# Optimization experiments

Hardware: AMD Instinct MI355X
Metric: run time of the kernel (lower is better)

Reference implementation:

```python
import jax, jax.numpy as jnp
import numpy as np

N, P, K, H, W = 16, 2048, 512, 256, 256
ZTHRESH = 2.0          # PRUN_ZSCORE_THRESHOLD
MULT = 5               # HV_HYPOTHESIS_IN_MASK_MULTIPLIER


def setup_inputs() -> dict:
    key = jax.random.key(0)
    uv_img = jax.random.normal(key, (N, 2, H, W), dtype=jnp.float32)
    rng = np.random.default_rng(0)
    # mask points per instance (torch.where(mask[i]) made fixed-shape)
    pts = rng.integers(0, H, size=(N, P, 2)).astype(np.int32)
    # multinomial pair sampling without replacement: distinct indices per pair
    i0 = rng.integers(0, P, size=(N, K))
    off = rng.integers(1, P, size=(N, K))
    i1 = (i0 + off) % P
    pair_idx = np.stack([i0, i1], axis=-1).astype(np.int32)
    return {"uv_img": uv_img, "pts": jnp.asarray(pts), "pair_idx": jnp.asarray(pair_idx)}


def _gather_uv(uv_img, coords):
    # uv_img: [N,2,H,W], coords: [N,M,2] int -> [N,M,2] uv values
    n, _, h, w = uv_img.shape
    flat = coords[..., 0] * w + coords[..., 1]            # [N,M]
    uv_flat = uv_img.reshape(n, 2, h * w)                 # [N,2,HW]
    g = jnp.take_along_axis(uv_flat, flat[:, None, :], axis=2)  # [N,2,M]
    return jnp.transpose(g, (0, 2, 1))                    # [N,M,2]


def reference(uv_img, pts, pair_idx):
    # --- generate hypotheses (batched pinverse solver) ---
    p0 = jnp.take_along_axis(pts, pair_idx[..., 0:1], axis=1)  # [N,K,2]
    p1 = jnp.take_along_axis(pts, pair_idx[..., 1:2], axis=1)  # [N,K,2]
    uv0 = _gather_uv(uv_img, p0)                               # [N,K,2]
    uv1 = _gather_uv(uv_img, p1)                               # [N,K,2]
    A = jnp.stack((uv0, -uv1), axis=-1)                        # [N,K,2,2]
    Bv = (p1 - p0).astype(jnp.float32)[..., None]              # [N,K,2,1]  (-p0 + p1)
    X = jnp.matmul(jnp.linalg.pinv(A), Bv)                     # [N,K,2,1]
    x0 = X[:, :, 0, :]                                         # [N,K,1]
    Y = x0 * uv0 + p0.astype(jnp.float32)                      # [N,K,2] hypotheses

    # --- prune outliers (z-score, drop -> nan in torch; here masked) ---
    mean = jnp.mean(Y, axis=1, keepdims=True)
    std = jnp.std(Y, axis=1, keepdims=True, ddof=1)
    z = jnp.abs((Y - mean) / std)
    bad = jnp.any(z > ZTHRESH, axis=-1) | jnp.any(jnp.isnan(Y), axis=-1)  # [N,K]
    Yz = jnp.where(bad[..., None], 0.0, Y)                     # nan-hypotheses zeroed (as torch does)

    # --- hypothesis weights ---
    ptsf = pts.astype(jnp.float32)                             # [N,P,2]
    uv_p = _gather_uv(uv_img, pts)                             # [N,P,2]
    d = Y[:, :, None, :] - ptsf[:, None, :, :]                 # [N,K,P,2]
    a = d / jnp.linalg.norm(d, axis=-1, keepdims=True)
    b = jnp.einsum('nkpc,npc->nkp', a, uv_p) > 0               # direction agreement
    w = jnp.sum(b, axis=-1)                                    # [N,K] int
    match = Y.astype(jnp.int32)[:, :, None, :] == pts[:, None, :, :]
    h_in_mask = jnp.sum(match[..., 0] & match[..., 1], axis=-1)  # [N,K]
    factor = jnp.where(h_in_mask == 1, MULT, 1)
    w = (factor * w).astype(jnp.float32)
    w = jnp.where(bad, 0.0, w)                                 # outlier rows get 0 weight
    w = w / jnp.maximum(jnp.sum(w, axis=1, keepdims=True), 1.0)

    weighted_mean = jnp.sum(Yz * w[..., None], axis=1)         # [N,2]
    pixel_xy = weighted_mean[:, ::-1]                          # (row,col) -> (x,y)
    return pixel_xy
```

## Files before the change

kernel.cpp:

```cpp
#include <hip/hip_runtime.h>
#include <math.h>

#define N_ 16
#define P_ 2048
#define K_ 512
#define H_ 256
#define W_ 256
#define ZTHRESH_ 2.0f

__global__ __launch_bounds__(256) void k1_gather(
    const float* __restrict__ uv_img, const int* __restrict__ pts,
    const int* __restrict__ pair, float* __restrict__ Y,
    float* __restrict__ uvp) {
  int id = blockIdx.x * 256 + threadIdx.x;
  if (id < N_ * P_) {
    int n = id / P_, p = id % P_;
    int c0 = pts[(n * P_ + p) * 2 + 0];
    int c1 = pts[(n * P_ + p) * 2 + 1];
    const float* base = uv_img + (size_t)n * 2 * H_ * W_;
    uvp[(n * P_ + p) * 2 + 0] = base[c0 * W_ + c1];
    uvp[(n * P_ + p) * 2 + 1] = base[H_ * W_ + c0 * W_ + c1];
  } else {
    int j = id - N_ * P_;
    if (j < N_ * K_) {
      int n = j / K_, k = j % K_;
      int i0 = pair[(n * K_ + k) * 2 + 0];
      int i1 = pair[(n * K_ + k) * 2 + 1];
      int p0y = pts[(n * P_ + i0) * 2 + 0], p0x = pts[(n * P_ + i0) * 2 + 1];
      int p1y = pts[(n * P_ + i1) * 2 + 0], p1x = pts[(n * P_ + i1) * 2 + 1];
      const float* base = uv_img + (size_t)n * 2 * H_ * W_;
      float u00 = base[p0y * W_ + p0x];
      float u01 = base[H_ * W_ + p0y * W_ + p0x];
      float u10 = base[p1y * W_ + p1x];
      float u11 = base[H_ * W_ + p1y * W_ + p1x];
      float B0 = (float)(p1y - p0y);
      float B1 = (float)(p1x - p0x);
      float det = u10 * u01 - u00 * u11;
      float x0 = (u10 * B1 - B0 * u11) / det;
      Y[(n * K_ + k) * 2 + 0] = x0 * u00 + (float)p0y;
      Y[(n * K_ + k) * 2 + 1] = x0 * u01 + (float)p0x;
    }
  }
}

__global__ __launch_bounds__(512) void k2_stats(
    const float* __restrict__ Y, int* __restrict__ bad,
    int* __restrict__ wcnt, int* __restrict__ hcnt) {
  int n = blockIdx.x;
  int tid = threadIdx.x;
  float y0 = Y[(n * K_ + tid) * 2 + 0];
  float y1 = Y[(n * K_ + tid) * 2 + 1];
  wcnt[n * K_ + tid] = 0;
  hcnt[n * K_ + tid] = 0;

  __shared__ float lds[8][2];
  __shared__ float mean0s, mean1s, std0s, std1s;
  int wave = tid >> 6, lane = tid & 63;

  float a0 = y0, a1 = y1;
  for (int off = 32; off >= 1; off >>= 1) {
    a0 += __shfl_down(a0, off);
    a1 += __shfl_down(a1, off);
  }
  if (lane == 0) { lds[wave][0] = a0; lds[wave][1] = a1; }
  __syncthreads();
  if (tid == 0) {
    float t0 = 0.f, t1 = 0.f;
    for (int i = 0; i < 8; i++) { t0 += lds[i][0]; t1 += lds[i][1]; }
    mean0s = t0 / (float)K_;
    mean1s = t1 / (float)K_;
  }
  __syncthreads();
  float m0 = mean0s, m1 = mean1s;
  float e0 = y0 - m0, e1 = y1 - m1;

  a0 = e0 * e0; a1 = e1 * e1;
  for (int off = 32; off >= 1; off >>= 1) {
    a0 += __shfl_down(a0, off);
    a1 += __shfl_down(a1, off);
  }
  __syncthreads();
  if (lane == 0) { lds[wave][0] = a0; lds[wave][1] = a1; }
  __syncthreads();
  if (tid == 0) {
    float t0 = 0.f, t1 = 0.f;
    for (int i = 0; i < 8; i++) { t0 += lds[i][0]; t1 += lds[i][1]; }
    std0s = sqrtf(t0 / (float)(K_ - 1));
    std1s = sqrtf(t1 / (float)(K_ - 1));
  }
  __syncthreads();
  float z0 = fabsf(e0 / std0s), z1 = fabsf(e1 / std1s);
  int b = (z0 > ZTHRESH_) | (z1 > ZTHRESH_) | (y0 != y0) | (y1 != y1);
  bad[n * K_ + tid] = b;
}

__global__ __launch_bounds__(256) void k3_votes(
    const float* __restrict__ Y, const int* __restrict__ pts,
    const float* __restrict__ uvp, int* __restrict__ wcnt,
    int* __restrict__ hcnt) {
  int b = blockIdx.x;
  int n = b >> 4;
  int kt = (b >> 3) & 1;
  int pt = b & 7;
  int tid = threadIdx.x;

  __shared__ float4 sf[256];
  __shared__ int2 si[256];

  int p = pt * 256 + tid;
  int py = pts[(n * P_ + p) * 2 + 0];
  int px = pts[(n * P_ + p) * 2 + 1];
  float u = uvp[(n * P_ + p) * 2 + 0];
  float v = uvp[(n * P_ + p) * 2 + 1];
  sf[tid] = make_float4((float)py, (float)px, u, v);
  si[tid] = make_int2(py, px);
  __syncthreads();

  int k = kt * 256 + tid;
  float y0 = Y[(n * K_ + k) * 2 + 0];
  float y1 = Y[(n * K_ + k) * 2 + 1];
  int iy0 = (int)y0, iy1 = (int)y1;
  int cnt = 0, hm = 0;
#pragma unroll 4
  for (int i = 0; i < 256; i++) {
    float4 f = sf[i];
    int2 ii = si[i];
    float d0 = y0 - f.x;
    float d1 = y1 - f.y;
    float dot = d0 * f.z + d1 * f.w;
    cnt += (dot > 0.f) ? 1 : 0;
    hm += ((iy0 == ii.x) & (iy1 == ii.y)) ? 1 : 0;
  }
  atomicAdd(&wcnt[n * K_ + k], cnt);
  atomicAdd(&hcnt[n * K_ + k], hm);
}

__global__ __launch_bounds__(512) void k4_out(
    const float* __restrict__ Y, const int* __restrict__ bad,
    const int* __restrict__ wcnt, const int* __restrict__ hcnt,
    float* __restrict__ out) {
  int n = blockIdx.x;
  int tid = threadIdx.x;
  float y0 = Y[(n * K_ + tid) * 2 + 0];
  float y1 = Y[(n * K_ + tid) * 2 + 1];
  int bd = bad[n * K_ + tid];
  float w = (float)wcnt[n * K_ + tid];
  if (hcnt[n * K_ + tid] == 1) w *= 5.0f;
  if (bd) w = 0.f;
  float yz0 = bd ? 0.f : y0;
  float yz1 = bd ? 0.f : y1;
  float sw = w, s0 = w * yz0, s1 = w * yz1;

  int wave = tid >> 6, lane = tid & 63;
  __shared__ float lds[8][3];
  for (int off = 32; off >= 1; off >>= 1) {
    sw += __shfl_down(sw, off);
    s0 += __shfl_down(s0, off);
    s1 += __shfl_down(s1, off);
  }
  if (lane == 0) { lds[wave][0] = sw; lds[wave][1] = s0; lds[wave][2] = s1; }
  __syncthreads();
  if (tid == 0) {
    float tw = 0.f, t0 = 0.f, t1 = 0.f;
    for (int i = 0; i < 8; i++) {
      tw += lds[i][0]; t0 += lds[i][1]; t1 += lds[i][2];
    }
    float denom = fmaxf(tw, 1.0f);
    out[n * 2 + 0] = t1 / denom;
    out[n * 2 + 1] = t0 / denom;
  }
}

extern "C" void kernel_launch(void* const* d_in, const int* in_sizes, int n_in,
                              void* d_out, int out_size, void* d_ws,
                              size_t ws_size, hipStream_t stream) {
  const float* uv_img = (const float*)d_in[0];
  const int* pts = (const int*)d_in[1];
  const int* pair = (const int*)d_in[2];
  float* out = (float*)d_out;

  float* Y = (float*)d_ws;
  float* uvp = Y + N_ * K_ * 2;
  int* bad = (int*)(uvp + N_ * P_ * 2);
  int* wcnt = bad + N_ * K_;
  int* hcnt = wcnt + N_ * K_;

  hipLaunchKernelGGL(k1_gather, dim3((N_ * P_ + N_ * K_) / 256), dim3(256), 0,
                     stream, uv_img, pts, pair, Y, uvp);
  hipLaunchKernelGGL(k2_stats, dim3(N_), dim3(K_), 0, stream, Y, bad, wcnt,
                     hcnt);
  hipLaunchKernelGGL(k3_votes, dim3(256), dim3(256), 0, stream, Y, pts, uvp,
                     wcnt, hcnt);
  hipLaunchKernelGGL(k4_out, dim3(N_), dim3(K_), 0, stream, Y, bad, wcnt, hcnt,
                     out);
}
```

Before: 26.55 us.

## Fuse four kernels into two with a last-block-done final reduction

The gather, z-score stats, vote counting and final weighted mean were four launches; they become two. Zeroing of the counters and done flags moves into the gather kernel. The stats blocks now run next to the vote blocks in one grid, and the last of each instance's 17 blocks, found through an atomic counter, does the final reduction. This removes two launch and serialization gaps, at the cost of threadfence and atomic overhead and more complex synchronization.

Result: slower. 38.60 us (+45.3%).

```diff
diff --git a/kernel.cpp b/kernel.cpp
--- a/kernel.cpp
+++ b/kernel.cpp
@@ -8,166 +8,177 @@
 #define W_ 256
 #define ZTHRESH_ 2.0f
 
-__global__ __launch_bounds__(256) void k1_gather(
+__global__ __launch_bounds__(256) void kA(
     const float* __restrict__ uv_img, const int* __restrict__ pts,
     const int* __restrict__ pair, float* __restrict__ Y,
-    float* __restrict__ uvp) {
+    float* __restrict__ uvp, int* __restrict__ wcnt, int* __restrict__ hcnt,
+    int* __restrict__ done) {
   int id = blockIdx.x * 256 + threadIdx.x;
   if (id < N_ * P_) {
-    int n = id / P_, p = id % P_;
-    int c0 = pts[(n * P_ + p) * 2 + 0];
-    int c1 = pts[(n * P_ + p) * 2 + 1];
+    int n = id >> 11, p = id & (P_ - 1);
+    int2 c = ((const int2*)pts)[n * P_ + p];
     const float* base = uv_img + (size_t)n * 2 * H_ * W_;
-    uvp[(n * P_ + p) * 2 + 0] = base[c0 * W_ + c1];
-    uvp[(n * P_ + p) * 2 + 1] = base[H_ * W_ + c0 * W_ + c1];
-  } else {
-    int j = id - N_ * P_;
-    if (j < N_ * K_) {
-      int n = j / K_, k = j % K_;
-      int i0 = pair[(n * K_ + k) * 2 + 0];
-      int i1 = pair[(n * K_ + k) * 2 + 1];
-      int p0y = pts[(n * P_ + i0) * 2 + 0], p0x = pts[(n * P_ + i0) * 2 + 1];
-      int p1y = pts[(n * P_ + i1) * 2 + 0], p1x = pts[(n * P_ + i1) * 2 + 1];
-      const float* base = uv_img + (size_t)n * 2 * H_ * W_;
-      float u00 = base[p0y * W_ + p0x];
-      float u01 = base[H_ * W_ + p0y * W_ + p0x];
-      float u10 = base[p1y * W_ + p1x];
-      float u11 = base[H_ * W_ + p1y * W_ + p1x];
-      float B0 = (float)(p1y - p0y);
-      float B1 = (float)(p1x - p0x);
-      float det = u10 * u01 - u00 * u11;
-      float x0 = (u10 * B1 - B0 * u11) / det;
-      Y[(n * K_ + k) * 2 + 0] = x0 * u00 + (float)p0y;
-      Y[(n * K_ + k) * 2 + 1] = x0 * u01 + (float)p0x;
-    }
-  }
+    float2 g;
+    g.x = base[c.x * W_ + c.y];
+    g.y = base[H_ * W_ + c.x * W_ + c.y];
+    ((float2*)uvp)[n * P_ + p] = g;
+    return;
+  }
+  id -= N_ * P_;
+  if (id < N_ * K_) {
+    int n = id >> 9, k = id & (K_ - 1);
+    int2 pr = ((const int2*)pair)[n * K_ + k];
+    int2 p0 = ((const int2*)pts)[n * P_ + pr.x];
+    int2 p1 = ((const int2*)pts)[n * P_ + pr.y];
+    const float* base = uv_img + (size_t)n * 2 * H_ * W_;
+    float u00 = base[p0.x * W_ + p0.y];
+    float u01 = base[H_ * W_ + p0.x * W_ + p0.y];
+    float u10 = base[p1.x * W_ + p1.y];
+    float u11 = base[H_ * W_ + p1.x * W_ + p1.y];
+    float B0 = (float)(p1.x - p0.x);
+    float B1 = (float)(p1.y - p0.y);
+    float det = u10 * u01 - u00 * u11;
+    float x0 = (u10 * B1 - B0 * u11) / det;
+    float2 y;
+    y.x = x0 * u00 + (float)p0.x;
+    y.y = x0 * u01 + (float)p0.y;
+    ((float2*)Y)[n * K_ + k] = y;
+    return;
+  }
+  id -= N_ * K_;
+  if (id < N_ * K_) {
+    wcnt[id] = 0;
+    hcnt[id] = 0;
+    return;
+  }
+  id -= N_ * K_;
+  if (id < N_) done[id] = 0;
 }
 
-__global__ __launch_bounds__(512) void k2_stats(
-    const float* __restrict__ Y, int* __restrict__ bad,
-    int* __restrict__ wcnt, int* __restrict__ hcnt) {
-  int n = blockIdx.x;
-  int tid = threadIdx.x;
-  float y0 = Y[(n * K_ + tid) * 2 + 0];
-  float y1 = Y[(n * K_ + tid) * 2 + 1];
-  wcnt[n * K_ + tid] = 0;
-  hcnt[n * K_ + tid] = 0;
-
-  __shared__ float lds[8][2];
-  __shared__ float mean0s, mean1s, std0s, std1s;
-  int wave = tid >> 6, lane = tid & 63;
-
-  float a0 = y0, a1 = y1;
-  for (int off = 32; off >= 1; off >>= 1) {
-    a0 += __shfl_down(a0, off);
-    a1 += __shfl_down(a1, off);
-  }
-  if (lane == 0) { lds[wave][0] = a0; lds[wave][1] = a1; }
-  __syncthreads();
-  if (tid == 0) {
-    float t0 = 0.f, t1 = 0.f;
-    for (int i = 0; i < 8; i++) { t0 += lds[i][0]; t1 += lds[i][1]; }
-    mean0s = t0 / (float)K_;
-    mean1s = t1 / (float)K_;
-  }
-  __syncthreads();
-  float m0 = mean0s, m1 = mean1s;
-  float e0 = y0 - m0, e1 = y1 - m1;
-
-  a0 = e0 * e0; a1 = e1 * e1;
-  for (int off = 32; off >= 1; off >>= 1) {
-    a0 += __shfl_down(a0, off);
-    a1 += __shfl_down(a1, off);
-  }
-  __syncthreads();
-  if (lane == 0) { lds[wave][0] = a0; lds[wave][1] = a1; }
-  __syncthreads();
-  if (tid == 0) {
-    float t0 = 0.f, t1 = 0.f;
-    for (int i = 0; i < 8; i++) { t0 += lds[i][0]; t1 += lds[i][1]; }
-    std0s = sqrtf(t0 / (float)(K_ - 1));
-    std1s = sqrtf(t1 / (float)(K_ - 1));
-  }
-  __syncthreads();
-  float z0 = fabsf(e0 / std0s), z1 = fabsf(e1 / std1s);
-  int b = (z0 > ZTHRESH_) | (z1 > ZTHRESH_) | (y0 != y0) | (y1 != y1);
-  bad[n * K_ + tid] = b;
-}
-
-__global__ __launch_bounds__(256) void k3_votes(
-    const float* __restrict__ Y, const int* __restrict__ pts,
-    const float* __restrict__ uvp, int* __restrict__ wcnt,
-    int* __restrict__ hcnt) {
-  int b = blockIdx.x;
-  int n = b >> 4;
-  int kt = (b >> 3) & 1;
-  int pt = b & 7;
-  int tid = threadIdx.x;
-
+__global__ __launch_bounds__(256) void kB(
+    const int* __restrict__ pts, const float* __restrict__ Y,
+    const float* __restrict__ uvp, int* __restrict__ bad,
+    int* __restrict__ wcnt, int* __restrict__ hcnt, int* __restrict__ done,
+    float* __restrict__ out) {
+  int b = blockIdx.x, tid = threadIdx.x;
   __shared__ float4 sf[256];
   __shared__ int2 si[256];
-
-  int p = pt * 256 + tid;
-  int py = pts[(n * P_ + p) * 2 + 0];
-  int px = pts[(n * P_ + p) * 2 + 1];
-  float u = uvp[(n * P_ + p) * 2 + 0];
-  float v = uvp[(n * P_ + p) * 2 + 1];
-  sf[tid] = make_float4((float)py, (float)px, u, v);
-  si[tid] = make_int2(py, px);
+  __shared__ float red[4][3];
+  __shared__ float m0s, m1s, sd0s, sd1s;
+  __shared__ int s_old;
+  int wave = tid >> 6, lane = tid & 63;
+  int n;
+
+  if (b < 256) {
+    n = b >> 4;
+    int kt = (b >> 3) & 1, pt = b & 7;
+    int p = pt * 256 + tid;
+    int2 pc = ((const int2*)pts)[n * P_ + p];
+    float2 uc = ((const float2*)uvp)[n * P_ + p];
+    sf[tid] = make_float4((float)pc.x, (float)pc.y, uc.x, uc.y);
+    si[tid] = pc;
+    __syncthreads();
+
+    int k = kt * 256 + tid;
+    float2 y = ((const float2*)Y)[n * K_ + k];
+    int iy0 = (int)y.x, iy1 = (int)y.y;
+    int cnt = 0, hm = 0;
+#pragma unroll 4
+    for (int i = 0; i < 256; i++) {
+      float4 f = sf[i];
+      int2 ii = si[i];
+      float d0 = y.x - f.x;
+      float d1 = y.y - f.y;
+      float dot = d0 * f.z + d1 * f.w;
+      cnt += (dot > 0.f) ? 1 : 0;
+      hm += ((iy0 == ii.x) & (iy1 == ii.y)) ? 1 : 0;
+    }
+    atomicAdd(&wcnt[n * K_ + k], cnt);
+    atomicAdd(&hcnt[n * K_ + k], hm);
+  } else {
+    n = b - 256;
+    float2 ya = ((const float2*)Y)[n * K_ + tid];
+    float2 yb = ((const float2*)Y)[n * K_ + tid + 256];
+    float a0 = ya.x + yb.x, a1 = ya.y + yb.y;
+    for (int off = 32; off >= 1; off >>= 1) {
+      a0 += __shfl_down(a0, off);
+      a1 += __shfl_down(a1, off);
+    }
+    if (lane == 0) { red[wave][0] = a0; red[wave][1] = a1; }
+    __syncthreads();
+    if (tid == 0) {
+      float t0 = red[0][0] + red[1][0] + red[2][0] + red[3][0];
+      float t1 = red[0][1] + red[1][1] + red[2][1] + red[3][1];
+      m0s = t0 / (float)K_;
+      m1s = t1 / (float)K_;
+    }
+    __syncthreads();
+    float m0 = m0s, m1 = m1s;
+    float ea0 = ya.x - m0, ea1 = ya.y - m1;
+    float eb0 = yb.x - m0, eb1 = yb.y - m1;
+    a0 = ea0 * ea0 + eb0 * eb0;
+    a1 = ea1 * ea1 + eb1 * eb1;
+    for (int off = 32; off >= 1; off >>= 1) {
+      a0 += __shfl_down(a0, off);
+      a1 += __shfl_down(a1, off);
+    }
+    __syncthreads();
+    if (lane == 0) { red[wave][0] = a0; red[wave][1] = a1; }
+    __syncthreads();
+    if (tid == 0) {
+      float t0 = red[0][0] + red[1][0] + red[2][0] + red[3][0];
+      float t1 = red[0][1] + red[1][1] + red[2][1] + red[3][1];
+      sd0s = sqrtf(t0 / (float)(K_ - 1));
+      sd1s = sqrtf(t1 / (float)(K_ - 1));
+    }
+    __syncthreads();
+    float sd0 = sd0s, sd1 = sd1s;
+    int bda = (fabsf(ea0 / sd0) > ZTHRESH_) | (fabsf(ea1 / sd1) > ZTHRESH_) |
+              (ya.x != ya.x) | (ya.y != ya.y);
+    int bdb = (fabsf(eb0 / sd0) > ZTHRESH_) | (fabsf(eb1 / sd1) > ZTHRESH_) |
+              (yb.x != yb.x) | (yb.y != yb.y);
+    bad[n * K_ + tid] = bda;
+    bad[n * K_ + tid + 256] = bdb;
+  }
+
+  __threadfence();
   __syncthreads();
-
-  int k = kt * 256 + tid;
-  float y0 = Y[(n * K_ + k) * 2 + 0];
-  float y1 = Y[(n * K_ + k) * 2 + 1];
-  int iy0 = (int)y0, iy1 = (int)y1;
-  int cnt = 0, hm = 0;
-#pragma unroll 4
-  for (int i = 0; i < 256; i++) {
-    float4 f = sf[i];
-    int2 ii = si[i];
-    float d0 = y0 - f.x;
-    float d1 = y1 - f.y;
-    float dot = d0 * f.z + d1 * f.w;
-    cnt += (dot > 0.f) ? 1 : 0;
-    hm += ((iy0 == ii.x) & (iy1 == ii.y)) ? 1 : 0;
-  }
-  atomicAdd(&wcnt[n * K_ + k], cnt);
-  atomicAdd(&hcnt[n * K_ + k], hm);
-}
-
-__global__ __launch_bounds__(512) void k4_out(
-    const float* __restrict__ Y, const int* __restrict__ bad,
-    const int* __restrict__ wcnt, const int* __restrict__ hcnt,
-    float* __restrict__ out) {
-  int n = blockIdx.x;
-  int tid = threadIdx.x;
-  float y0 = Y[(n * K_ + tid) * 2 + 0];
-  float y1 = Y[(n * K_ + tid) * 2 + 1];
-  int bd = bad[n * K_ + tid];
-  float w = (float)wcnt[n * K_ + tid];
-  if (hcnt[n * K_ + tid] == 1) w *= 5.0f;
-  if (bd) w = 0.f;
-  float yz0 = bd ? 0.f : y0;
-  float yz1 = bd ? 0.f : y1;
-  float sw = w, s0 = w * yz0, s1 = w * yz1;
-
-  int wave = tid >> 6, lane = tid & 63;
-  __shared__ float lds[8][3];
-  for (int off = 32; off >= 1; off >>= 1) {
-    sw += __shfl_down(sw, off);
-    s0 += __shfl_down(s0, off);
-    s1 += __shfl_down(s1, off);
-  }
-  if (lane == 0) { lds[wave][0] = sw; lds[wave][1] = s0; lds[wave][2] = s1; }
+  if (tid == 0)
+    s_old = __hip_atomic_fetch_add(&done[n], 1, __ATOMIC_ACQ_REL,
+                                   __HIP_MEMORY_SCOPE_AGENT);
   __syncthreads();
-  if (tid == 0) {
-    float tw = 0.f, t0 = 0.f, t1 = 0.f;
-    for (int i = 0; i < 8; i++) {
-      tw += lds[i][0]; t0 += lds[i][1]; t1 += lds[i][2];
-    }
-    float denom = fmaxf(tw, 1.0f);
-    out[n * 2 + 0] = t1 / denom;
-    out[n * 2 + 1] = t0 / denom;
+  if (s_old == 16) {
+    float sw = 0.f, s0 = 0.f, s1 = 0.f;
+    for (int kk = tid; kk < K_; kk += 256) {
+      float2 y = ((const float2*)Y)[n * K_ + kk];
+      int bd = __hip_atomic_load(&bad[n * K_ + kk], __ATOMIC_RELAXED,
+                                 __HIP_MEMORY_SCOPE_AGENT);
+      int wc = __hip_atomic_load(&wcnt[n * K_ + kk], __ATOMIC_RELAXED,
+                                 __HIP_MEMORY_SCOPE_AGENT);
+      int hc = __hip_atomic_load(&hcnt[n * K_ + kk], __ATOMIC_RELAXED,
+                                 __HIP_MEMORY_SCOPE_AGENT);
+      float w = (float)wc * ((hc == 1) ? 5.0f : 1.0f);
+      if (bd) w = 0.f;
+      sw += w;
+      s0 += w * (bd ? 0.f : y.x);
+      s1 += w * (bd ? 0.f : y.y);
+    }
+    for (int off = 32; off >= 1; off >>= 1) {
+      sw += __shfl_down(sw, off);
+      s0 += __shfl_down(s0, off);
+      s1 += __shfl_down(s1, off);
+    }
+    __syncthreads();
+    if (lane == 0) { red[wave][0] = sw; red[wave][1] = s0; red[wave][2] = s1; }
+    __syncthreads();
+    if (tid == 0) {
+      float tw = red[0][0] + red[1][0] + red[2][0] + red[3][0];
+      float t0 = red[0][1] + red[1][1] + red[2][1] + red[3][1];
+      float t1 = red[0][2] + red[1][2] + red[2][2] + red[3][2];
+      float den = fmaxf(tw, 1.0f);
+      out[n * 2 + 0] = t1 / den;
+      out[n * 2 + 1] = t0 / den;
+    }
   }
 }
 
@@ -184,13 +195,11 @@
   int* bad = (int*)(uvp + N_ * P_ * 2);
   int* wcnt = bad + N_ * K_;
   int* hcnt = wcnt + N_ * K_;
-
-  hipLaunchKernelGGL(k1_gather, dim3((N_ * P_ + N_ * K_) / 256), dim3(256), 0,
-                     stream, uv_img, pts, pair, Y, uvp);
-  hipLaunchKernelGGL(k2_stats, dim3(N_), dim3(K_), 0, stream, Y, bad, wcnt,
-                     hcnt);
-  hipLaunchKernelGGL(k3_votes, dim3(256), dim3(256), 0, stream, Y, pts, uvp,
-                     wcnt, hcnt);
-  hipLaunchKernelGGL(k4_out, dim3(N_), dim3(K_), 0, stream, Y, bad, wcnt, hcnt,
-                     out);
+  int* done = hcnt + N_ * K_;
+
+  int itemsA = N_ * P_ + N_ * K_ + N_ * K_ + N_;
+  hipLaunchKernelGGL(kA, dim3((itemsA + 255) / 256), dim3(256), 0, stream,
+                     uv_img, pts, pair, Y, uvp, wcnt, hcnt, done);
+  hipLaunchKernelGGL(kB, dim3(272), dim3(256), 0, stream, pts, Y, uvp, bad,
+                     wcnt, hcnt, done, out);
 }
```

## Fuse gather, stats, voting and reduction into one kernel plus tiny final

Applied to the files above, without the earlier changes.

Replaces four kernels with a main kernel where each block recomputes all hypotheses and z-score stats for its instance in LDS, then votes for its 32-hypothesis slice against all points, and a small final kernel reduces per-block partials. This removes three launches, the global Y/uvp/bad/count round-trips and the atomics. In exchange, each instance's hypothesis generation and statistics are computed redundantly by 16 blocks, and the per-point uv values are gathered inside the voting loop.

Result: slower. 28.73 us (+8.2%).

```diff
diff --git a/kernel.cpp b/kernel.cpp
--- a/kernel.cpp
+++ b/kernel.cpp
@@ -6,168 +6,160 @@
 #define K_ 512
 #define H_ 256
 #define W_ 256
-#define ZTHRESH_ 2.0f
+#define HW_ (H_ * W_)
+#define ZT_ 2.0f
 
-__global__ __launch_bounds__(256) void k1_gather(
+__global__ __launch_bounds__(512) void hough_main(
     const float* __restrict__ uv_img, const int* __restrict__ pts,
-    const int* __restrict__ pair, float* __restrict__ Y,
-    float* __restrict__ uvp) {
-  int id = blockIdx.x * 256 + threadIdx.x;
-  if (id < N_ * P_) {
-    int n = id / P_, p = id % P_;
-    int c0 = pts[(n * P_ + p) * 2 + 0];
-    int c1 = pts[(n * P_ + p) * 2 + 1];
-    const float* base = uv_img + (size_t)n * 2 * H_ * W_;
-    uvp[(n * P_ + p) * 2 + 0] = base[c0 * W_ + c1];
-    uvp[(n * P_ + p) * 2 + 1] = base[H_ * W_ + c0 * W_ + c1];
-  } else {
-    int j = id - N_ * P_;
-    if (j < N_ * K_) {
-      int n = j / K_, k = j % K_;
-      int i0 = pair[(n * K_ + k) * 2 + 0];
-      int i1 = pair[(n * K_ + k) * 2 + 1];
-      int p0y = pts[(n * P_ + i0) * 2 + 0], p0x = pts[(n * P_ + i0) * 2 + 1];
-      int p1y = pts[(n * P_ + i1) * 2 + 0], p1x = pts[(n * P_ + i1) * 2 + 1];
-      const float* base = uv_img + (size_t)n * 2 * H_ * W_;
-      float u00 = base[p0y * W_ + p0x];
-      float u01 = base[H_ * W_ + p0y * W_ + p0x];
-      float u10 = base[p1y * W_ + p1x];
-      float u11 = base[H_ * W_ + p1y * W_ + p1x];
-      float B0 = (float)(p1y - p0y);
-      float B1 = (float)(p1x - p0x);
-      float det = u10 * u01 - u00 * u11;
-      float x0 = (u10 * B1 - B0 * u11) / det;
-      Y[(n * K_ + k) * 2 + 0] = x0 * u00 + (float)p0y;
-      Y[(n * K_ + k) * 2 + 1] = x0 * u01 + (float)p0x;
-    }
+    const int* __restrict__ pair, float4* __restrict__ partial) {
+  int b = blockIdx.x;
+  int n = b >> 4, kt = b & 15;
+  int tid = threadIdx.x;
+  int lane = tid & 63, wave = tid >> 6;
+
+  __shared__ float2 Ys[K_];
+  __shared__ float4 sf[256];
+  __shared__ int2 si[256];
+  __shared__ unsigned char badf[K_];
+  __shared__ float red[8][3];
+  __shared__ float bc[4];
+
+  const int2* pts2 = (const int2*)pts + n * P_;
+  const float* base = uv_img + (size_t)n * 2 * HW_;
+
+  {
+    int2 pr = ((const int2*)pair)[n * K_ + tid];
+    int2 p0 = pts2[pr.x];
+    int2 p1 = pts2[pr.y];
+    float u00 = base[p0.x * W_ + p0.y];
+    float u01 = base[HW_ + p0.x * W_ + p0.y];
+    float u10 = base[p1.x * W_ + p1.y];
+    float u11 = base[HW_ + p1.x * W_ + p1.y];
+    float B0 = (float)(p1.x - p0.x);
+    float B1 = (float)(p1.y - p0.y);
+    float det = u10 * u01 - u00 * u11;
+    float x0 = (u10 * B1 - B0 * u11) / det;
+    Ys[tid] = make_float2(x0 * u00 + (float)p0.x, x0 * u01 + (float)p0.y);
   }
-}
+  __syncthreads();
 
-__global__ __launch_bounds__(512) void k2_stats(
-    const float* __restrict__ Y, int* __restrict__ bad,
-    int* __restrict__ wcnt, int* __restrict__ hcnt) {
-  int n = blockIdx.x;
-  int tid = threadIdx.x;
-  float y0 = Y[(n * K_ + tid) * 2 + 0];
-  float y1 = Y[(n * K_ + tid) * 2 + 1];
-  wcnt[n * K_ + tid] = 0;
-  hcnt[n * K_ + tid] = 0;
-
-  __shared__ float lds[8][2];
-  __shared__ float mean0s, mean1s, std0s, std1s;
-  int wave = tid >> 6, lane = tid & 63;
-
-  float a0 = y0, a1 = y1;
+  float2 y = Ys[tid];
+  float a0 = y.x, a1 = y.y;
   for (int off = 32; off >= 1; off >>= 1) {
     a0 += __shfl_down(a0, off);
     a1 += __shfl_down(a1, off);
   }
-  if (lane == 0) { lds[wave][0] = a0; lds[wave][1] = a1; }
+  if (lane == 0) { red[wave][0] = a0; red[wave][1] = a1; }
   __syncthreads();
   if (tid == 0) {
     float t0 = 0.f, t1 = 0.f;
-    for (int i = 0; i < 8; i++) { t0 += lds[i][0]; t1 += lds[i][1]; }
-    mean0s = t0 / (float)K_;
-    mean1s = t1 / (float)K_;
+    for (int i = 0; i < 8; i++) { t0 += red[i][0]; t1 += red[i][1]; }
+    bc[0] = t0 / (float)K_;
+    bc[1] = t1 / (float)K_;
   }
   __syncthreads();
-  float m0 = mean0s, m1 = mean1s;
-  float e0 = y0 - m0, e1 = y1 - m1;
-
-  a0 = e0 * e0; a1 = e1 * e1;
+  float m0 = bc[0], m1 = bc[1];
+  float e0 = y.x - m0, e1 = y.y - m1;
+  a0 = e0 * e0;
+  a1 = e1 * e1;
   for (int off = 32; off >= 1; off >>= 1) {
     a0 += __shfl_down(a0, off);
     a1 += __shfl_down(a1, off);
   }
-  __syncthreads();
-  if (lane == 0) { lds[wave][0] = a0; lds[wave][1] = a1; }
+  if (lane == 0) { red[wave][0] = a0; red[wave][1] = a1; }
   __syncthreads();
   if (tid == 0) {
     float t0 = 0.f, t1 = 0.f;
-    for (int i = 0; i < 8; i++) { t0 += lds[i][0]; t1 += lds[i][1]; }
-    std0s = sqrtf(t0 / (float)(K_ - 1));
-    std1s = sqrtf(t1 / (float)(K_ - 1));
+    for (int i = 0; i < 8; i++) { t0 += red[i][0]; t1 += red[i][1]; }
+    bc[2] = sqrtf(t0 / (float)(K_ - 1));
+    bc[3] = sqrtf(t1 / (float)(K_ - 1));
   }
   __syncthreads();
-  float z0 = fabsf(e0 / std0s), z1 = fabsf(e1 / std1s);
-  int b = (z0 > ZTHRESH_) | (z1 > ZTHRESH_) | (y0 != y0) | (y1 != y1);
-  bad[n * K_ + tid] = b;
+  float sd0 = bc[2], sd1 = bc[3];
+  int bd = (fabsf(e0 / sd0) > ZT_) | (fabsf(e1 / sd1) > ZT_) |
+           (y.x != y.x) | (y.y != y.y);
+  badf[tid] = (unsigned char)bd;
+
+  int k = kt * 32 + (tid >> 4);
+  int pl = tid & 15;
+  float2 yk = Ys[k];
+  int iy0 = (int)yk.x, iy1 = (int)yk.y;
+  int cnt = 0, hm = 0;
+
+  for (int t = 0; t < 8; t++) {
+    __syncthreads();
+    int pp = tid & 255, ch = tid >> 8;
+    int p = t * 256 + pp;
+    int2 pc = pts2[p];
+    float g = base[ch * HW_ + pc.x * W_ + pc.y];
+    ((float*)&sf[pp])[2 + ch] = g;
+    if (ch == 0) {
+      ((float*)&sf[pp])[0] = (float)pc.x;
+      ((float*)&sf[pp])[1] = (float)pc.y;
+      si[pp] = pc;
+    }
+    __syncthreads();
+#pragma unroll 4
+    for (int i = 0; i < 16; i++) {
+      int idx = pl + 16 * i;
+      float4 f = sf[idx];
+      int2 ii = si[idx];
+      float d0 = yk.x - f.x;
+      float d1 = yk.y - f.y;
+      float dot = d0 * f.z + d1 * f.w;
+      cnt += (dot > 0.f) ? 1 : 0;
+      hm += ((iy0 == ii.x) & (iy1 == ii.y)) ? 1 : 0;
+    }
+  }
+
+  for (int off = 8; off >= 1; off >>= 1) {
+    cnt += __shfl_down(cnt, off);
+    hm += __shfl_down(hm, off);
+  }
+  float w = 0.f, s0 = 0.f, s1 = 0.f;
+  if (pl == 0) {
+    if (badf[k]) {
+      w = 0.f;
+    } else {
+      w = (float)cnt * ((hm == 1) ? 5.0f : 1.0f);
+      s0 = w * yk.x;
+      s1 = w * yk.y;
+    }
+  }
+  for (int off = 32; off >= 1; off >>= 1) {
+    w += __shfl_down(w, off);
+    s0 += __shfl_down(s0, off);
+    s1 += __shfl_down(s1, off);
+  }
+  __syncthreads();
+  if (lane == 0) { red[wave][0] = w; red[wave][1] = s0; red[wave][2] = s1; }
+  __syncthreads();
+  if (tid == 0) {
+    float tw = 0.f, t0 = 0.f, t1 = 0.f;
+    for (int i = 0; i < 8; i++) {
+      tw += red[i][0];
+      t0 += red[i][1];
+      t1 += red[i][2];
+    }
+    partial[b] = make_float4(tw, t0, t1, 0.f);
+  }
 }
 
-__global__ __launch_bounds__(256) void k3_votes(
-    const float* __restrict__ Y, const int* __restrict__ pts,
-    const float* __restrict__ uvp, int* __restrict__ wcnt,
-    int* __restrict__ hcnt) {
-  int b = blockIdx.x;
-  int n = b >> 4;
-  int kt = (b >> 3) & 1;
-  int pt = b & 7;
+__global__ __launch_bounds__(256) void hough_final(
+    const float4* __restrict__ partial, float* __restrict__ out) {
   int tid = threadIdx.x;
-
-  __shared__ float4 sf[256];
-  __shared__ int2 si[256];
-
-  int p = pt * 256 + tid;
-  int py = pts[(n * P_ + p) * 2 + 0];
-  int px = pts[(n * P_ + p) * 2 + 1];
-  float u = uvp[(n * P_ + p) * 2 + 0];
-  float v = uvp[(n * P_ + p) * 2 + 1];
-  sf[tid] = make_float4((float)py, (float)px, u, v);
-  si[tid] = make_int2(py, px);
-  __syncthreads();
-
-  int k = kt * 256 + tid;
-  float y0 = Y[(n * K_ + k) * 2 + 0];
-  float y1 = Y[(n * K_ + k) * 2 + 1];
-  int iy0 = (int)y0, iy1 = (int)y1;
-  int cnt = 0, hm = 0;
-#pragma unroll 4
-  for (int i = 0; i < 256; i++) {
-    float4 f = sf[i];
-    int2 ii = si[i];
-    float d0 = y0 - f.x;
-    float d1 = y1 - f.y;
-    float dot = d0 * f.z + d1 * f.w;
-    cnt += (dot > 0.f) ? 1 : 0;
-    hm += ((iy0 == ii.x) & (iy1 == ii.y)) ? 1 : 0;
-  }
-  atomicAdd(&wcnt[n * K_ + k], cnt);
-  atomicAdd(&hcnt[n * K_ + k], hm);
-}
-
-__global__ __launch_bounds__(512) void k4_out(
-    const float* __restrict__ Y, const int* __restrict__ bad,
-    const int* __restrict__ wcnt, const int* __restrict__ hcnt,
-    float* __restrict__ out) {
-  int n = blockIdx.x;
-  int tid = threadIdx.x;
-  float y0 = Y[(n * K_ + tid) * 2 + 0];
-  float y1 = Y[(n * K_ + tid) * 2 + 1];
-  int bd = bad[n * K_ + tid];
-  float w = (float)wcnt[n * K_ + tid];
-  if (hcnt[n * K_ + tid] == 1) w *= 5.0f;
-  if (bd) w = 0.f;
-  float yz0 = bd ? 0.f : y0;
-  float yz1 = bd ? 0.f : y1;
-  float sw = w, s0 = w * yz0, s1 = w * yz1;
-
-  int wave = tid >> 6, lane = tid & 63;
-  __shared__ float lds[8][3];
-  for (int off = 32; off >= 1; off >>= 1) {
+  float4 p = partial[tid];
+  float sw = p.x, s0 = p.y, s1 = p.z;
+  for (int off = 8; off >= 1; off >>= 1) {
     sw += __shfl_down(sw, off);
     s0 += __shfl_down(s0, off);
     s1 += __shfl_down(s1, off);
   }
-  if (lane == 0) { lds[wave][0] = sw; lds[wave][1] = s0; lds[wave][2] = s1; }
-  __syncthreads();
-  if (tid == 0) {
-    float tw = 0.f, t0 = 0.f, t1 = 0.f;
-    for (int i = 0; i < 8; i++) {
-      tw += lds[i][0]; t0 += lds[i][1]; t1 += lds[i][2];
-    }
-    float denom = fmaxf(tw, 1.0f);
-    out[n * 2 + 0] = t1 / denom;
-    out[n * 2 + 1] = t0 / denom;
+  if ((tid & 15) == 0) {
+    int n = tid >> 4;
+    float den = fmaxf(sw, 1.0f);
+    out[n * 2 + 0] = s1 / den;
+    out[n * 2 + 1] = s0 / den;
   }
 }
 
@@ -178,19 +170,9 @@
   const int* pts = (const int*)d_in[1];
   const int* pair = (const int*)d_in[2];
   float* out = (float*)d_out;
+  float4* partial = (float4*)d_ws;
 
-  float* Y = (float*)d_ws;
-  float* uvp = Y + N_ * K_ * 2;
-  int* bad = (int*)(uvp + N_ * P_ * 2);
-  int* wcnt = bad + N_ * K_;
-  int* hcnt = wcnt + N_ * K_;
-
-  hipLaunchKernelGGL(k1_gather, dim3((N_ * P_ + N_ * K_) / 256), dim3(256), 0,
-                     stream, uv_img, pts, pair, Y, uvp);
-  hipLaunchKernelGGL(k2_stats, dim3(N_), dim3(K_), 0, stream, Y, bad, wcnt,
-                     hcnt);
-  hipLaunchKernelGGL(k3_votes, dim3(256), dim3(256), 0, stream, Y, pts, uvp,
-                     wcnt, hcnt);
-  hipLaunchKernelGGL(k4_out, dim3(N_), dim3(K_), 0, stream, Y, bad, wcnt, hcnt,
-                     out);
+  hipLaunchKernelGGL(hough_main, dim3(256), dim3(512), 0, stream, uv_img, pts,
+                     pair, partial);
+  hipLaunchKernelGGL(hough_final, dim3(1), dim3(256), 0, stream, partial, out);
 }
```
